# Kernel tuning notes

Hardware: AMD Instinct MI355X
Metric: run time of the kernel (lower is better)

## Reference

```python
import jax, jax.numpy as jnp
import numpy as np

THRESHOLD = 0.9
DECAY = 0.6


def setup_inputs() -> dict:
    key = jax.random.key(0)
    k1, k2, k3 = jax.random.split(key, 3)
    T, B, I, H, O = 100, 256, 784, 1024, 10
    # binary-ish spike input (rand fill, thresholded to emulate Poisson spikes)
    x = (jax.random.uniform(k1, (T, B, I)) < 0.3).astype(jnp.float32)
    W1 = 0.01 * jax.random.normal(k2, (I, H), dtype=jnp.float32)
    W2 = 0.01 * jax.random.normal(k3, (H, O), dtype=jnp.float32)
    return {"input_spikes_time": x, "W1": W1, "W2": W2}


def reference(input_spikes_time, W1, W2):
    T, B, _ = input_spikes_time.shape
    H = W1.shape[1]
    O = W2.shape[1]
    dt = input_spikes_time.dtype

    def lif(mem, current):
        # mem = mem*decay + I; spike if mem >= threshold; soft reset
        mem = mem * DECAY + current
        spikes = (mem >= THRESHOLD).astype(dt)
        mem = mem - spikes * THRESHOLD
        return mem, spikes

    def step(carry, x_t):
        mem1, mem2 = carry
        hidden_u = x_t @ W1                 # [B, H]
        mem1, hidden_spikes = lif(mem1, hidden_u)
        output_u = hidden_spikes @ W2       # [B, O]
        mem2, output_spikes = lif(mem2, output_u)
        return (mem1, mem2), (hidden_spikes, output_spikes)

    init = (jnp.zeros((B, H), dt), jnp.zeros((B, O), dt))
    _, (hidden_all, output_all) = jax.lax.scan(step, init, input_spikes_time)
    return hidden_all, output_all
```

## Files before the change

### kernel.cpp

```cpp
#include <hip/hip_runtime.h>
#include <hip/hip_bf16.h>

#define T_STEPS 100
#define BATCH   256
#define IN_DIM  784
#define HID_DIM 1024
#define OUT_DIM 10
#define M_ROWS  (T_STEPS * BATCH)
#define KPAD    800
#define NT      25
#define STG     12288
#define DECAY   0.6f
#define THRESH  0.9f

typedef __attribute__((ext_vector_type(8))) short bf16x8;
typedef __attribute__((ext_vector_type(4))) float f32x4;

#define PACK8(dstp, v0, v1)                                                                        \
    {                                                                                              \
        unsigned int p0 = __builtin_amdgcn_perm(__builtin_bit_cast(unsigned int, (v0).y),          \
                                                __builtin_bit_cast(unsigned int, (v0).x), 0x07060302u); \
        unsigned int p1 = __builtin_amdgcn_perm(__builtin_bit_cast(unsigned int, (v0).w),          \
                                                __builtin_bit_cast(unsigned int, (v0).z), 0x07060302u); \
        unsigned int p2 = __builtin_amdgcn_perm(__builtin_bit_cast(unsigned int, (v1).y),          \
                                                __builtin_bit_cast(unsigned int, (v1).x), 0x07060302u); \
        unsigned int p3 = __builtin_amdgcn_perm(__builtin_bit_cast(unsigned int, (v1).w),          \
                                                __builtin_bit_cast(unsigned int, (v1).z), 0x07060302u); \
        *(uint4*)(dstp) = make_uint4(p0, p1, p2, p3);                                              \
    }

#define GLL(g, l)                                                                                  \
    __builtin_amdgcn_global_load_lds((const __attribute__((address_space(1))) void*)(g),           \
                                     (__attribute__((address_space(3))) void*)(l), 16, 0, 0)

__device__ __forceinline__ void w1_split_body(const float* __restrict__ W1,
                                              unsigned short* __restrict__ Th,
                                              unsigned short* __restrict__ Tl,
                                              int b2, int t,
                                              unsigned short lh[32][33],
                                              unsigned short ll[32][33]) {
    const int nb = (b2 & 31) * 32;
    const int kb = (b2 >> 5) * 32;
    const int ln = t & 31, lk = t >> 5;
    #pragma unroll
    for (int i = 0; i < 4; ++i) {
        const int k = kb + lk + i * 8;
        const float w = (k < IN_DIM) ? W1[(size_t)k * HID_DIM + nb + ln] : 0.f;
        __hip_bfloat16 h = __float2bfloat16(w);
        float hf = __bfloat162float(h);
        __hip_bfloat16 l = __float2bfloat16(w - hf);
        lh[lk + i * 8][ln] = __builtin_bit_cast(unsigned short, h);
        ll[lk + i * 8][ln] = __builtin_bit_cast(unsigned short, l);
    }
    __syncthreads();
    const int o_n = t >> 3;
    const int o_k = (t & 7) * 4;
    ushort4 vh, vl;
    vh.x = lh[o_k + 0][o_n]; vh.y = lh[o_k + 1][o_n];
    vh.z = lh[o_k + 2][o_n]; vh.w = lh[o_k + 3][o_n];
    vl.x = ll[o_k + 0][o_n]; vl.y = ll[o_k + 1][o_n];
    vl.z = ll[o_k + 2][o_n]; vl.w = ll[o_k + 3][o_n];
    *(ushort4*)&Th[(size_t)(nb + o_n) * KPAD + kb + o_k] = vh;
    *(ushort4*)&Tl[(size_t)(nb + o_n) * KPAD + kb + o_k] = vl;
}

__global__ __launch_bounds__(256) void prep(const float* __restrict__ X,
                                            const float* __restrict__ W1,
                                            unsigned short* __restrict__ Xb,
                                            unsigned short* __restrict__ Th,
                                            unsigned short* __restrict__ Tl,
                                            float* __restrict__ outu) {
    __shared__ unsigned short lh[32][33];
    __shared__ unsigned short ll[32][33];
    const int bid = blockIdx.x;
    const int t   = threadIdx.x;

    if (bid < 10000) {
        const int gid = bid * 256 + t;
        const int r   = gid / 100;
        const int c   = gid - r * 100;
        unsigned short* dst = Xb + (size_t)r * KPAD + c * 8;
        if (c < 98) {
            const float* s = X + (size_t)r * IN_DIM + c * 8;
            float4 v0 = *(const float4*)s, v1 = *(const float4*)(s + 4);
            PACK8(dst, v0, v1);
        } else {
            *(uint4*)dst = make_uint4(0u, 0u, 0u, 0u);
        }
    } else if (bid < 10800) {
        w1_split_body(W1, Th, Tl, bid - 10000, t, lh, ll);
    } else {
        float4* p = (float4*)outu;
        p[(bid - 10800) * 256 + t] = make_float4(0.f, 0.f, 0.f, 0.f);
    }
}

__global__ __launch_bounds__(256) void prep_small(const float* __restrict__ W1,
                                                  unsigned short* __restrict__ Th,
                                                  unsigned short* __restrict__ Tl,
                                                  float* __restrict__ outu) {
    __shared__ unsigned short lh[32][33];
    __shared__ unsigned short ll[32][33];
    const int bid = blockIdx.x;
    const int t   = threadIdx.x;
    if (bid < 800) {
        w1_split_body(W1, Th, Tl, bid, t, lh, ll);
    } else {
        float4* p = (float4*)outu;
        p[(bid - 800) * 256 + t] = make_float4(0.f, 0.f, 0.f, 0.f);
    }
}

__global__ __launch_bounds__(256, 2) void gemm1_pipe(const unsigned short* __restrict__ Xb,
                                                     const unsigned short* __restrict__ Th,
                                                     const unsigned short* __restrict__ Tl,
                                                     float* __restrict__ C) {
    __shared__ unsigned short smem[3 * STG];

    const int tid = threadIdx.x;
    const int bid = blockIdx.x;
    const int xcd = bid & 7;
    const int j_  = bid >> 3;
    const int m0  = (xcd * 25 + (j_ >> 3)) * 128;
    const int n0  = (j_ & 7) * 128;

    const int lane = tid & 63, wv = tid >> 6;
    const int wm   = (wv & 1) * 64, wn = (wv >> 1) * 64;
    const int ml   = lane & 15, quad = lane >> 4;

    const int row  = tid >> 2;
    const int slot = tid & 3;
    const int sOff = (slot ^ ((row >> 1) & 3)) * 8;

    const unsigned short* gA0 = Xb + (size_t)(m0 + row)      * KPAD + sOff;
    const unsigned short* gA1 = Xb + (size_t)(m0 + row + 64) * KPAD + sOff;
    const unsigned short* gH0 = Th + (size_t)(n0 + row)      * KPAD + sOff;
    const unsigned short* gH1 = Th + (size_t)(n0 + row + 64) * KPAD + sOff;
    const unsigned short* gL0 = Tl + (size_t)(n0 + row)      * KPAD + sOff;
    const unsigned short* gL1 = Tl + (size_t)(n0 + row + 64) * KPAD + sOff;

#define STAGE(bf, it)                                                     \
    {                                                                     \
        unsigned short* b_ = smem + (bf) * STG;                           \
        const int k_ = (it) * 32;                                         \
        GLL(gA0 + k_, b_ + tid * 8);                                      \
        GLL(gA1 + k_, b_ + 2048 + tid * 8);                               \
        GLL(gH0 + k_, b_ + 4096 + tid * 8);                               \
        GLL(gH1 + k_, b_ + 6144 + tid * 8);                               \
        GLL(gL0 + k_, b_ + 8192 + tid * 8);                               \
        GLL(gL1 + k_, b_ + 10240 + tid * 8);                              \
    }

    f32x4 acc[4][4];
    #pragma unroll
    for (int i = 0; i < 4; ++i)
        #pragma unroll
        for (int j = 0; j < 4; ++j)
            acc[i][j] = (f32x4){0.f, 0.f, 0.f, 0.f};

    int offA[4], offB[4];
    #pragma unroll
    for (int i = 0; i < 4; ++i) {
        const int m = wm + i * 16 + ml;
        offA[i] = m * 32 + ((quad ^ ((m >> 1) & 3)) * 8);
    }
    #pragma unroll
    for (int j = 0; j < 4; ++j) {
        const int n = wn + j * 16 + ml;
        offB[j] = n * 32 + ((quad ^ ((n >> 1) & 3)) * 8);
    }

    STAGE(0, 0);
    STAGE(1, 1);

    int buf = 0;
    for (int it = 0; it < NT; ++it) {
        if (it < NT - 1) asm volatile("s_waitcnt vmcnt(6)" ::: "memory");
        else             asm volatile("s_waitcnt vmcnt(0)" ::: "memory");
        __builtin_amdgcn_s_barrier();
        asm volatile("" ::: "memory");

        if (it + 2 < NT) {
            int nb = buf + 2; if (nb >= 3) nb -= 3;
            STAGE(nb, it + 2);
        }

        const unsigned short* base = smem + buf * STG;
        bf16x8 af[4], bh[4], bl[4];
        #pragma unroll
        for (int i = 0; i < 4; ++i)
            af[i] = *(const bf16x8*)&base[offA[i]];
        #pragma unroll
        for (int j = 0; j < 4; ++j) {
            bh[j] = *(const bf16x8*)&base[4096 + offB[j]];
            bl[j] = *(const bf16x8*)&base[8192 + offB[j]];
        }

        __builtin_amdgcn_s_setprio(1);
        #pragma unroll
        for (int i = 0; i < 4; ++i)
            #pragma unroll
            for (int j = 0; j < 4; ++j) {
                acc[i][j] = __builtin_amdgcn_mfma_f32_16x16x32_bf16(af[i], bh[j], acc[i][j], 0, 0, 0);
                acc[i][j] = __builtin_amdgcn_mfma_f32_16x16x32_bf16(af[i], bl[j], acc[i][j], 0, 0, 0);
            }
        __builtin_amdgcn_s_setprio(0);

        buf = (buf == 2) ? 0 : buf + 1;
    }
#undef STAGE

    #pragma unroll
    for (int i = 0; i < 4; ++i)
        #pragma unroll
        for (int j = 0; j < 4; ++j) {
            const int r0 = m0 + wm + i * 16 + quad * 4;
            const int c0 = n0 + wn + j * 16 + ml;
            #pragma unroll
            for (int r = 0; r < 4; ++r)
                C[(size_t)(r0 + r) * HID_DIM + c0] = acc[i][j][r];
        }
}

__global__ __launch_bounds__(256, 3) void gemm1_fallback(const float* __restrict__ X,
                                                         const unsigned short* __restrict__ Th,
                                                         const unsigned short* __restrict__ Tl,
                                                         float* __restrict__ C) {
    __shared__ unsigned short As[128 * 32];
    __shared__ unsigned short Bhs[128 * 32];
    __shared__ unsigned short Bls[128 * 32];

    const int tid = threadIdx.x;
    const int bid = blockIdx.x;
    const int xcd = bid & 7;
    const int j_  = bid >> 3;
    const int m0  = (xcd * 25 + (j_ >> 3)) * 128;
    const int n0  = (j_ & 7) * 128;

    const int lane = tid & 63, wv = tid >> 6;
    const int wm   = (wv & 1) * 64, wn = (wv >> 1) * 64;
    const int ml   = lane & 15, quad = lane >> 4;

    const int sr = tid >> 2;
    const int sc = tid & 3;
    const int f0 = (sr >> 1) & 3;
    const int w0 = sr * 32 + ((sc ^ f0) * 8);
    const int w1 = (sr + 64) * 32 + ((sc ^ f0) * 8);

    const float*          Xa = X  + (size_t)(m0 + sr)      * IN_DIM + sc * 8;
    const float*          Xc = X  + (size_t)(m0 + sr + 64) * IN_DIM + sc * 8;
    const unsigned short* Ha = Th + (size_t)(n0 + sr)      * KPAD   + sc * 8;
    const unsigned short* Hb = Th + (size_t)(n0 + sr + 64) * KPAD   + sc * 8;
    const unsigned short* La = Tl + (size_t)(n0 + sr)      * KPAD   + sc * 8;
    const unsigned short* Lb = Tl + (size_t)(n0 + sr + 64) * KPAD   + sc * 8;

    f32x4 acc[4][4];
    #pragma unroll
    for (int i = 0; i < 4; ++i)
        #pragma unroll
        for (int j = 0; j < 4; ++j)
            acc[i][j] = (f32x4){0.f, 0.f, 0.f, 0.f};

    float4 xa0 = *(const float4*)&Xa[0], xa1 = *(const float4*)&Xa[4];
    float4 xb0 = *(const float4*)&Xc[0], xb1 = *(const float4*)&Xc[4];
    uint4  vh0 = *(const uint4*)&Ha[0],  vh1 = *(const uint4*)&Hb[0];
    uint4  vl0 = *(const uint4*)&La[0],  vl1 = *(const uint4*)&Lb[0];
    PACK8(&As[w0], xa0, xa1);
    PACK8(&As[w1], xb0, xb1);
    *(uint4*)&Bhs[w0] = vh0;  *(uint4*)&Bhs[w1] = vh1;
    *(uint4*)&Bls[w0] = vl0;  *(uint4*)&Bls[w1] = vl1;
    __syncthreads();

    for (int it = 0; it < NT; ++it) {
        bf16x8 af[4], bh[4], bl[4];
        #pragma unroll
        for (int i = 0; i < 4; ++i) {
            const int m = wm + i * 16 + ml;
            af[i] = *(const bf16x8*)&As[m * 32 + ((quad ^ ((m >> 1) & 3)) * 8)];
        }
        #pragma unroll
        for (int j = 0; j < 4; ++j) {
            const int n   = wn + j * 16 + ml;
            const int idx = n * 32 + ((quad ^ ((n >> 1) & 3)) * 8);
            bh[j] = *(const bf16x8*)&Bhs[idx];
            bl[j] = *(const bf16x8*)&Bls[idx];
        }

        const bool have_next = (it + 1 < NT);
        if (have_next) {
            const int kt = (it + 1) * 32;
            const int c0 = kt + sc * 8;
            const bool v0 = (c0 < IN_DIM), v1 = (c0 + 4 < IN_DIM);
            xa0 = v0 ? *(const float4*)&Xa[kt]     : make_float4(0.f, 0.f, 0.f, 0.f);
            xa1 = v1 ? *(const float4*)&Xa[kt + 4] : make_float4(0.f, 0.f, 0.f, 0.f);
            xb0 = v0 ? *(const float4*)&Xc[kt]     : make_float4(0.f, 0.f, 0.f, 0.f);
            xb1 = v1 ? *(const float4*)&Xc[kt + 4] : make_float4(0.f, 0.f, 0.f, 0.f);
            vh0 = *(const uint4*)&Ha[kt];  vh1 = *(const uint4*)&Hb[kt];
            vl0 = *(const uint4*)&La[kt];  vl1 = *(const uint4*)&Lb[kt];
        }

        #pragma unroll
        for (int i = 0; i < 4; ++i)
            #pragma unroll
            for (int j = 0; j < 4; ++j) {
                acc[i][j] = __builtin_amdgcn_mfma_f32_16x16x32_bf16(af[i], bh[j], acc[i][j], 0, 0, 0);
                acc[i][j] = __builtin_amdgcn_mfma_f32_16x16x32_bf16(af[i], bl[j], acc[i][j], 0, 0, 0);
            }

        __syncthreads();
        if (have_next) {
            PACK8(&As[w0], xa0, xa1);
            PACK8(&As[w1], xb0, xb1);
            *(uint4*)&Bhs[w0] = vh0;  *(uint4*)&Bhs[w1] = vh1;
            *(uint4*)&Bls[w0] = vl0;  *(uint4*)&Bls[w1] = vl1;
            __syncthreads();
        }
    }

    #pragma unroll
    for (int i = 0; i < 4; ++i)
        #pragma unroll
        for (int j = 0; j < 4; ++j) {
            const int r0 = m0 + wm + i * 16 + quad * 4;
            const int c0 = n0 + wn + j * 16 + ml;
            #pragma unroll
            for (int r = 0; r < 4; ++r)
                C[(size_t)(r0 + r) * HID_DIM + c0] = acc[i][j][r];
        }
}

__global__ __launch_bounds__(256) void lif1_fused(float* __restrict__ hid,
                                                  const float* __restrict__ W2,
                                                  float* __restrict__ outu) {
    const int idx = blockIdx.x * blockDim.x + threadIdx.x;
    float2* h2 = (float2*)hid;
    const int stride2 = (BATCH * HID_DIM) / 2;
    const int b  = idx >> 9;
    const int h0 = (idx * 2) & 1023;

    float2 mem = make_float2(0.f, 0.f);
    float2 u[4];
    #pragma unroll
    for (int c = 0; c < 4; ++c) u[c] = h2[c * stride2 + idx];

    for (int t = 0; t < T_STEPS; t += 4) {
        float2 nu[4];
        if (t + 4 < T_STEPS) {
            #pragma unroll
            for (int c = 0; c < 4; ++c) nu[c] = h2[(t + 4 + c) * stride2 + idx];
        }
        #pragma unroll
        for (int c = 0; c < 4; ++c) {
            float2 uu = u[c];
            float2 s;
            mem.x = mem.x * DECAY + uu.x; s.x = (mem.x >= THRESH) ? 1.f : 0.f; mem.x -= s.x * THRESH;
            mem.y = mem.y * DECAY + uu.y; s.y = (mem.y >= THRESH) ? 1.f : 0.f; mem.y -= s.y * THRESH;
            h2[(t + c) * stride2 + idx] = s;
            if (s.x + s.y > 0.f) {
                float* od = outu + (size_t)(t + c) * (BATCH * OUT_DIM) + b * OUT_DIM;
                #pragma unroll
                for (int e = 0; e < 2; ++e) {
                    const float sv = (&s.x)[e];
                    if (sv != 0.f) {
                        const float* w = W2 + (size_t)(h0 + e) * OUT_DIM;
                        #pragma unroll
                        for (int o = 0; o < OUT_DIM; ++o) atomicAdd(&od[o], w[o]);
                    }
                }
            }
        }
        #pragma unroll
        for (int c = 0; c < 4; ++c) u[c] = nu[c];
    }
}

__global__ __launch_bounds__(256) void lif2(float* __restrict__ outp) {
    const int n = blockIdx.x * blockDim.x + threadIdx.x;
    const int stride = BATCH * OUT_DIM;
    if (n >= stride) return;
    float mem = 0.f;
    float u[4];
    #pragma unroll
    for (int c = 0; c < 4; ++c) u[c] = outp[c * stride + n];
    for (int t = 0; t < T_STEPS; t += 4) {
        float nu[4];
        if (t + 4 < T_STEPS) {
            #pragma unroll
            for (int c = 0; c < 4; ++c) nu[c] = outp[(t + 4 + c) * stride + n];
        }
        #pragma unroll
        for (int c = 0; c < 4; ++c) {
            mem = mem * DECAY + u[c];
            float s = (mem >= THRESH) ? 1.f : 0.f;
            mem -= s * THRESH;
            outp[(t + c) * stride + n] = s;
        }
        #pragma unroll
        for (int c = 0; c < 4; ++c) u[c] = nu[c];
    }
}

extern "C" void kernel_launch(void* const* d_in, const int* in_sizes, int n_in,
                              void* d_out, int out_size, void* d_ws, size_t ws_size,
                              hipStream_t stream) {
    const float* x  = (const float*)d_in[0];
    const float* W1 = (const float*)d_in[1];
    const float* W2 = (const float*)d_in[2];
    float* out  = (float*)d_out;
    float* hid  = out;
    float* outu = out + (size_t)M_ROWS * HID_DIM;

    unsigned short* Th = (unsigned short*)d_ws;
    unsigned short* Tl = Th + (size_t)HID_DIM * KPAD;
    unsigned short* Xb = Tl + (size_t)HID_DIM * KPAD;

    const size_t ws_needed_big =
        (size_t)2 * HID_DIM * KPAD * sizeof(unsigned short) +
        (size_t)M_ROWS * KPAD * sizeof(unsigned short);

    if (ws_size >= ws_needed_big) {
        prep<<<11050, 256, 0, stream>>>(x, W1, Xb, Th, Tl, outu);
        gemm1_pipe<<<1600, 256, 0, stream>>>(Xb, Th, Tl, hid);
    } else {
        prep_small<<<1050, 256, 0, stream>>>(W1, Th, Tl, outu);
        gemm1_fallback<<<1600, 256, 0, stream>>>(x, Th, Tl, hid);
    }

    lif1_fused<<<(BATCH * HID_DIM / 2) / 256, 256, 0, stream>>>(hid, W2, outu);

    lif2<<<(BATCH * OUT_DIM + 255) / 256, 256, 0, stream>>>(outu);
}
```

Baseline: 278.4 us.

## Load GEMM1 B operands straight into registers, keep only A in LDS

The bf16 hi/lo W1 tiles are no longer staged through shared memory. Each lane now loads its B fragments directly from global memory into double-buffered registers one iteration ahead. Only the activation tile A stays in LDS, now in a 4-slot ring staged three iterations ahead. The smaller LDS footprint allows a launch bound of 3 blocks per CU instead of 2, which is meant to cut LDS traffic and raise occupancy. In exchange, B is read from global memory per wave with strided 16-byte accesses, relying on cache hits, and register pressure goes up.

```diff
diff --git a/kernel.cpp b/kernel.cpp
--- a/kernel.cpp
+++ b/kernel.cpp
@@ -9,7 +9,7 @@
 #define M_ROWS  (T_STEPS * BATCH)
 #define KPAD    800
 #define NT      25
-#define STG     12288
+#define ASTG    4096
 #define DECAY   0.6f
 #define THRESH  0.9f
 
@@ -111,11 +111,11 @@
     }
 }
 
-__global__ __launch_bounds__(256, 2) void gemm1_pipe(const unsigned short* __restrict__ Xb,
+__global__ __launch_bounds__(256, 3) void gemm1_breg(const unsigned short* __restrict__ Xb,
                                                      const unsigned short* __restrict__ Th,
                                                      const unsigned short* __restrict__ Tl,
                                                      float* __restrict__ C) {
-    __shared__ unsigned short smem[3 * STG];
+    __shared__ unsigned short smem[4 * ASTG];
 
     const int tid = threadIdx.x;
     const int bid = blockIdx.x;
@@ -134,21 +134,14 @@
 
     const unsigned short* gA0 = Xb + (size_t)(m0 + row)      * KPAD + sOff;
     const unsigned short* gA1 = Xb + (size_t)(m0 + row + 64) * KPAD + sOff;
-    const unsigned short* gH0 = Th + (size_t)(n0 + row)      * KPAD + sOff;
-    const unsigned short* gH1 = Th + (size_t)(n0 + row + 64) * KPAD + sOff;
-    const unsigned short* gL0 = Tl + (size_t)(n0 + row)      * KPAD + sOff;
-    const unsigned short* gL1 = Tl + (size_t)(n0 + row + 64) * KPAD + sOff;
-
-#define STAGE(bf, it)                                                     \
-    {                                                                     \
-        unsigned short* b_ = smem + (bf) * STG;                           \
-        const int k_ = (it) * 32;                                         \
-        GLL(gA0 + k_, b_ + tid * 8);                                      \
-        GLL(gA1 + k_, b_ + 2048 + tid * 8);                               \
-        GLL(gH0 + k_, b_ + 4096 + tid * 8);                               \
-        GLL(gH1 + k_, b_ + 6144 + tid * 8);                               \
-        GLL(gL0 + k_, b_ + 8192 + tid * 8);                               \
-        GLL(gL1 + k_, b_ + 10240 + tid * 8);                              \
+
+    const unsigned short* pH[4];
+    const unsigned short* pL[4];
+    #pragma unroll
+    for (int j = 0; j < 4; ++j) {
+        const int n = n0 + wn + j * 16 + ml;
+        pH[j] = Th + (size_t)n * KPAD + quad * 8;
+        pL[j] = Tl + (size_t)n * KPAD + quad * 8;
     }
 
     f32x4 acc[4][4];
@@ -158,57 +151,69 @@
         for (int j = 0; j < 4; ++j)
             acc[i][j] = (f32x4){0.f, 0.f, 0.f, 0.f};
 
-    int offA[4], offB[4];
+    int offA[4];
     #pragma unroll
     for (int i = 0; i < 4; ++i) {
         const int m = wm + i * 16 + ml;
         offA[i] = m * 32 + ((quad ^ ((m >> 1) & 3)) * 8);
     }
-    #pragma unroll
-    for (int j = 0; j < 4; ++j) {
-        const int n = wn + j * 16 + ml;
-        offB[j] = n * 32 + ((quad ^ ((n >> 1) & 3)) * 8);
-    }
-
-    STAGE(0, 0);
-    STAGE(1, 1);
-
-    int buf = 0;
-    for (int it = 0; it < NT; ++it) {
-        if (it < NT - 1) asm volatile("s_waitcnt vmcnt(6)" ::: "memory");
-        else             asm volatile("s_waitcnt vmcnt(0)" ::: "memory");
+
+    auto stageA = [&](int it) __attribute__((always_inline)) {
+        unsigned short* b_ = smem + (it & 3) * ASTG;
+        const int ko = it * 32;
+        GLL(gA0 + ko, b_ + tid * 8);
+        GLL(gA1 + ko, b_ + 2048 + tid * 8);
+    };
+
+    auto loadB = [&](uint4 (&h)[4], uint4 (&l)[4], int it) __attribute__((always_inline)) {
+        const int ko = it * 32;
+        #pragma unroll
+        for (int j = 0; j < 4; ++j) {
+            h[j] = *(const uint4*)(pH[j] + ko);
+            l[j] = *(const uint4*)(pL[j] + ko);
+        }
+    };
+
+    uint4 b0h[4], b0l[4], b1h[4], b1l[4];
+
+    auto iter = [&](int k, uint4 (&ch)[4], uint4 (&cl)[4],
+                    uint4 (&nh)[4], uint4 (&nl)[4]) __attribute__((always_inline)) {
+        asm volatile("s_waitcnt vmcnt(12)" ::: "memory");
         __builtin_amdgcn_s_barrier();
         asm volatile("" ::: "memory");
 
-        if (it + 2 < NT) {
-            int nb = buf + 2; if (nb >= 3) nb -= 3;
-            STAGE(nb, it + 2);
-        }
-
-        const unsigned short* base = smem + buf * STG;
-        bf16x8 af[4], bh[4], bl[4];
+        if (k + 1 < NT) loadB(nh, nl, k + 1);
+        if (k + 3 < NT) stageA(k + 3);
+
+        const unsigned short* base = smem + (k & 3) * ASTG;
+        bf16x8 af[4];
         #pragma unroll
         for (int i = 0; i < 4; ++i)
             af[i] = *(const bf16x8*)&base[offA[i]];
-        #pragma unroll
-        for (int j = 0; j < 4; ++j) {
-            bh[j] = *(const bf16x8*)&base[4096 + offB[j]];
-            bl[j] = *(const bf16x8*)&base[8192 + offB[j]];
-        }
 
         __builtin_amdgcn_s_setprio(1);
         #pragma unroll
         for (int i = 0; i < 4; ++i)
             #pragma unroll
             for (int j = 0; j < 4; ++j) {
-                acc[i][j] = __builtin_amdgcn_mfma_f32_16x16x32_bf16(af[i], bh[j], acc[i][j], 0, 0, 0);
-                acc[i][j] = __builtin_amdgcn_mfma_f32_16x16x32_bf16(af[i], bl[j], acc[i][j], 0, 0, 0);
+                acc[i][j] = __builtin_amdgcn_mfma_f32_16x16x32_bf16(
+                    af[i], __builtin_bit_cast(bf16x8, ch[j]), acc[i][j], 0, 0, 0);
+                acc[i][j] = __builtin_amdgcn_mfma_f32_16x16x32_bf16(
+                    af[i], __builtin_bit_cast(bf16x8, cl[j]), acc[i][j], 0, 0, 0);
             }
         __builtin_amdgcn_s_setprio(0);
-
-        buf = (buf == 2) ? 0 : buf + 1;
-    }
-#undef STAGE
+    };
+
+    stageA(0);
+    stageA(1);
+    loadB(b0h, b0l, 0);
+    stageA(2);
+
+    for (int k = 0; k + 1 < NT; k += 2) {
+        iter(k,     b0h, b0l, b1h, b1l);
+        iter(k + 1, b1h, b1l, b0h, b0l);
+    }
+    iter(NT - 1, b0h, b0l, b1h, b1l);
 
     #pragma unroll
     for (int i = 0; i < 4; ++i)
@@ -420,7 +425,7 @@
 
     if (ws_size >= ws_needed_big) {
         prep<<<11050, 256, 0, stream>>>(x, W1, Xb, Th, Tl, outu);
-        gemm1_pipe<<<1600, 256, 0, stream>>>(Xb, Th, Tl, hid);
+        gemm1_breg<<<1600, 256, 0, stream>>>(Xb, Th, Tl, hid);
     } else {
         prep_small<<<1050, 256, 0, stream>>>(W1, Th, Tl, outu);
         gemm1_fallback<<<1600, 256, 0, stream>>>(x, Th, Tl, hid);
```

Measured after the change: 386.6 us. 1.39x slower.
